# Kernel tuning notes

Hardware: AMD Instinct MI355X
Metric: run time of the kernel (lower is better)

## Reference

```python
import jax, jax.numpy as jnp
import numpy as np
from jax import lax

B, N, M = 4, 4096, 4096
DK, DQ, DV, DT, H = 3, 3, 1, 1, 64


def _mlp(x, W1, b1, W2, b2):
    # Linear -> ReLU -> Linear (weights stored as [in, out])
    return jax.nn.relu(x @ W1 + b1) @ W2 + b2


def _l1_cdist(K, Q):
    # K: [B,N,H], Q: [B,M,H] -> [B,N,M] sum_h |k-q| without a B*N*M*H intermediate.
    def step(acc, kq):
        k, q = kq  # [B,N], [B,M]
        return acc + jnp.abs(k[:, :, None] - q[:, None, :]), None
    init = jnp.zeros((K.shape[0], K.shape[1], Q.shape[1]), K.dtype)
    acc, _ = lax.scan(step, init, (jnp.moveaxis(K, -1, 0), jnp.moveaxis(Q, -1, 0)))
    return acc


def setup_inputs() -> dict:
    key = jax.random.key(0)
    ks = jax.random.split(key, 20)

    def lin(k, fan_in, fan_out):
        bound = 1.0 / np.sqrt(fan_in)
        kw, kb = jax.random.split(k)
        W = jax.random.uniform(kw, (fan_in, fan_out), jnp.float32, -bound, bound)
        b = jax.random.uniform(kb, (fan_out,), jnp.float32, -bound, bound)
        return W, b

    Wk1, bk1 = lin(ks[0], DK, H)
    Wk2, bk2 = lin(ks[1], H, H)
    Wq1, bq1 = lin(ks[2], DQ, H)
    Wq2, bq2 = lin(ks[3], H, H)
    Wv1, bv1 = lin(ks[4], DV, H)
    Wv2, bv2 = lin(ks[5], H, H)
    Wo, bo = lin(ks[6], H, DT)

    return {
        "coords_f": jax.random.normal(ks[10], (B, N, DK), jnp.float32),
        "values_f": jax.random.normal(ks[11], (B, N, DV), jnp.float32),
        "coords_t": jax.random.normal(ks[12], (B, M, DQ), jnp.float32),
        "Wk1": Wk1, "bk1": bk1, "Wk2": Wk2, "bk2": bk2,
        "Wq1": Wq1, "bq1": bq1, "Wq2": Wq2, "bq2": bq2,
        "Wv1": Wv1, "bv1": bv1, "Wv2": Wv2, "bv2": bv2,
        "Wo": Wo, "bo": bo,
    }


def reference(coords_f, values_f, coords_t,
              Wk1, bk1, Wk2, bk2,
              Wq1, bq1, Wq2, bq2,
              Wv1, bv1, Wv2, bv2,
              Wo, bo):
    K = _mlp(coords_f, Wk1, bk1, Wk2, bk2)   # [B,N,H]
    Q = _mlp(coords_t, Wq1, bq1, Wq2, bq2)   # [B,M,H]
    V = _mlp(values_f, Wv1, bv1, Wv2, bv2)   # [B,N,H]
    score = _l1_cdist(K, Q)                  # [B,N,M]
    # Gaussian kernel on L1 distance, normalized over keys (dim=1 == N axis)
    attn = jax.nn.softmax(-(score ** 2) / 2.0, axis=1)   # [B,N,M]
    out = jnp.einsum('bnm,bnh->bmh', attn, V)            # [B,M,H]
    return out @ Wo + bo                                 # [B,M,DT]
```

## Files before the change

kernel.cpp:

```cpp
#include <hip/hip_runtime.h>
#include <math.h>

#define NPTS 4096
#define CC 0.7213475204444817f

__global__ __launch_bounds__(256) void feat_kernel(
    const float* __restrict__ coords, const float* __restrict__ W1,
    const float* __restrict__ b1, const float* __restrict__ W2,
    const float* __restrict__ b2, float* __restrict__ outT, int npts)
{
  __shared__ float sW1[3 * 64], sb1[64], sW2[64 * 64], sb2[64];
  const int tid = threadIdx.x;
  for (int i = tid; i < 192; i += 256) sW1[i] = W1[i];
  if (tid < 64) { sb1[tid] = b1[tid]; sb2[tid] = b2[tid]; }
  for (int i = tid; i < 4096; i += 256) sW2[i] = W2[i];
  __syncthreads();

  const int p  = blockIdx.x * 64 + (tid & 63);
  const int qh = (tid >> 6) * 16;
  if (p >= npts) return;
  const float c0 = coords[p * 3 + 0], c1 = coords[p * 3 + 1], c2 = coords[p * 3 + 2];

  float hid[64];
  #pragma unroll
  for (int j = 0; j < 64; ++j)
    hid[j] = fmaxf(0.f, fmaf(c0, sW1[j], fmaf(c1, sW1[64 + j], fmaf(c2, sW1[128 + j], sb1[j]))));

  float acc[16];
  #pragma unroll
  for (int h = 0; h < 16; ++h) acc[h] = sb2[qh + h];
  for (int j = 0; j < 64; ++j) {
    const float hj = hid[j];
    const float4* wrow = (const float4*)&sW2[j * 64 + qh];
    #pragma unroll
    for (int hq = 0; hq < 4; ++hq) {
      float4 wv = wrow[hq];
      acc[hq * 4 + 0] = fmaf(hj, wv.x, acc[hq * 4 + 0]);
      acc[hq * 4 + 1] = fmaf(hj, wv.y, acc[hq * 4 + 1]);
      acc[hq * 4 + 2] = fmaf(hj, wv.z, acc[hq * 4 + 2]);
      acc[hq * 4 + 3] = fmaf(hj, wv.w, acc[hq * 4 + 3]);
    }
  }
  const int b = p / NPTS, n = p % NPTS;
  #pragma unroll
  for (int h = 0; h < 16; ++h)
    outT[(size_t)(b * 64 + qh + h) * NPTS + n] = acc[h];
}

__global__ __launch_bounds__(256) void vo_kernel(
    const float* __restrict__ values, const float* __restrict__ Wv1,
    const float* __restrict__ bv1, const float* __restrict__ Wv2,
    const float* __restrict__ bv2, const float* __restrict__ Wo,
    float* __restrict__ VoOut, int npts)
{
  __shared__ float sWvO[64], sW1[64], sb1[64], sc0;
  const int tid = threadIdx.x;
  if (tid < 64) {
    float a = 0.f;
    for (int h = 0; h < 64; ++h) a = fmaf(Wv2[tid * 64 + h], Wo[h], a);
    sWvO[tid] = a;
    sW1[tid] = Wv1[tid];
    sb1[tid] = bv1[tid];
  } else if (tid == 64) {
    float a = 0.f;
    for (int h = 0; h < 64; ++h) a = fmaf(bv2[h], Wo[h], a);
    sc0 = a;
  }
  __syncthreads();
  const int p = blockIdx.x * 256 + tid;
  if (p >= npts) return;
  const float v = values[p];
  float a = sc0;
  #pragma unroll 8
  for (int j = 0; j < 64; ++j)
    a = fmaf(fmaxf(0.f, fmaf(v, sW1[j], sb1[j])), sWvO[j], a);
  VoOut[p] = a;
}

__global__ void __launch_bounds__(1024)
attn_kernel(
    const float* __restrict__ Kt, const float* __restrict__ Qt,
    const float* __restrict__ Vo, const float* __restrict__ bo,
    float* __restrict__ out)
{
  __shared__ float Qs[64 * 64];
  __shared__ float MtL[1024];
  __shared__ float numL[8192];
  __shared__ float denL[8192];

  const int b    = blockIdx.x >> 6;
  const int m0   = (blockIdx.x & 63) << 6;
  const int tid  = threadIdx.x;
  const int w    = tid >> 6;
  const int lane = tid & 63;
  const int lm = lane >> 3, ln = lane & 7;

  const float* __restrict__ KtB = Kt + (size_t)b * 64 * NPTS;
  const float* __restrict__ QtB = Qt + (size_t)b * 64 * NPTS;
  const float* __restrict__ VoB = Vo + (size_t)b * NPTS;

  {
    const int h = tid >> 4, c16 = (tid & 15) * 4;
    *(float4*)&Qs[h * 64 + c16] = *(const float4*)&QtB[(size_t)h * NPTS + m0 + c16];
    #pragma unroll
    for (int j = 0; j < 8; ++j) {
      numL[w * 512 + j * 64 + lane] = 0.f;
      denL[w * 512 + j * 64 + lane] = 0.f;
    }
  }
  __syncthreads();

  float acc[32];
  float Mt[8];
  #pragma unroll
  for (int x = 0; x < 32; ++x) acc[x] = 0.f;
  #pragma unroll
  for (int j = 0; j < 8; ++j) Mt[j] = __builtin_inff();

  const float* __restrict__ Kb = KtB + w * 32 + ln * 4;
  const float* __restrict__ Qb = &Qs[lm * 8];

  for (int I = 0; I < 8; ++I) {
    const float* __restrict__ Kn = Kb + I * 512;
    #pragma unroll 2
    for (int h = 0; h < 64; ++h) {
      float q[8], k[4];
      *(float4*)&k[0] = *(const float4*)(Kn + (size_t)h * NPTS);
      *(float4*)&q[0] = *(const float4*)(Qb + h * 64);
      *(float4*)&q[4] = *(const float4*)(Qb + h * 64 + 4);
      #pragma unroll
      for (int j = 0; j < 8; ++j) {
        #pragma unroll
        for (int i = 0; i < 4; i += 2) {
          float d0, d1;
          asm("v_sub_f32 %0, %4, %6\n\t"
              "v_sub_f32 %1, %5, %6\n\t"
              "v_add_f32 %2, %2, |%0|\n\t"
              "v_add_f32 %3, %3, |%1|"
              : "=&v"(d0), "=&v"(d1),
                "+v"(acc[j * 4 + i]), "+v"(acc[j * 4 + i + 1])
              : "v"(k[i]), "v"(k[i + 1]), "v"(q[j]));
        }
      }
    }

    {
      float vo[4];
      const int vb = I * 512 + w * 32 + ln * 4;
      *(float4*)&vo[0] = *(const float4*)&VoB[vb];
      #pragma unroll
      for (int j = 0; j < 8; ++j) {
        float rmin = fminf(fminf(acc[j*4+0], acc[j*4+1]), fminf(acc[j*4+2], acc[j*4+3]));
        rmin = fminf(rmin, __shfl_xor(rmin, 1));
        rmin = fminf(rmin, __shfl_xor(rmin, 2));
        rmin = fminf(rmin, __shfl_xor(rmin, 4));
        const float nM = fminf(Mt[j], rmin * rmin);
        const float sc = __builtin_amdgcn_exp2f(CC * (nM - Mt[j]));
        const int slot = w * 512 + j * 64 + lane;
        float nm = numL[slot] * sc;
        float dn = denL[slot] * sc;
        Mt[j] = nM;
        const float base = CC * nM;
        #pragma unroll
        for (int i = 0; i < 4; ++i) {
          const float a = acc[j * 4 + i];
          const float wgt = __builtin_amdgcn_exp2f(fmaf(-CC, a * a, base));
          dn += wgt;
          nm = fmaf(wgt, vo[i], nm);
          acc[j * 4 + i] = 0.f;
        }
        numL[slot] = nm;
        denL[slot] = dn;
      }
    }
  }

  if (ln == 0) {
    #pragma unroll
    for (int j = 0; j < 8; ++j)
      MtL[w * 64 + lm * 8 + j] = Mt[j];
  }
  __syncthreads();

  if (tid < 64) {
    const int m = tid;
    float M = __builtin_inff();
    #pragma unroll
    for (int ww = 0; ww < 16; ++ww) M = fminf(M, MtL[ww * 64 + m]);
    float Ns = 0.f, Ds = 0.f;
    #pragma unroll
    for (int ww = 0; ww < 16; ++ww) {
      const float f = __builtin_amdgcn_exp2f(CC * (M - MtL[ww * 64 + m]));
      float ns = 0.f, ds = 0.f;
      #pragma unroll
      for (int l = 0; l < 8; ++l) {
        ns += numL[ww * 512 + (m & 7) * 64 + (m >> 3) * 8 + l];
        ds += denL[ww * 512 + (m & 7) * 64 + (m >> 3) * 8 + l];
      }
      Ns = fmaf(ns, f, Ns);
      Ds = fmaf(ds, f, Ds);
    }
    out[(size_t)b * NPTS + m0 + m] = Ns / Ds + bo[0];
  }
}

extern "C" void kernel_launch(void* const* d_in, const int* in_sizes, int n_in,
                              void* d_out, int out_size, void* d_ws, size_t ws_size,
                              hipStream_t stream)
{
  const float* coords_f = (const float*)d_in[0];
  const float* values_f = (const float*)d_in[1];
  const float* coords_t = (const float*)d_in[2];
  const float* Wk1 = (const float*)d_in[3];
  const float* bk1 = (const float*)d_in[4];
  const float* Wk2 = (const float*)d_in[5];
  const float* bk2 = (const float*)d_in[6];
  const float* Wq1 = (const float*)d_in[7];
  const float* bq1 = (const float*)d_in[8];
  const float* Wq2 = (const float*)d_in[9];
  const float* bq2 = (const float*)d_in[10];
  const float* Wv1 = (const float*)d_in[11];
  const float* bv1 = (const float*)d_in[12];
  const float* Wv2 = (const float*)d_in[13];
  const float* bv2 = (const float*)d_in[14];
  const float* Wo  = (const float*)d_in[15];
  const float* bo  = (const float*)d_in[16];

  const int B    = in_sizes[0] / (NPTS * 3);
  const int npts = B * NPTS;

  float* Kt  = (float*)d_ws;
  float* Qt  = Kt + (size_t)B * 64 * NPTS;
  float* VoW = Qt + (size_t)B * 64 * NPTS;

  feat_kernel<<<npts / 64, 256, 0, stream>>>(coords_f, Wk1, bk1, Wk2, bk2, Kt, npts);
  feat_kernel<<<npts / 64, 256, 0, stream>>>(coords_t, Wq1, bq1, Wq2, bq2, Qt, npts);
  vo_kernel<<<npts / 256, 256, 0, stream>>>(values_f, Wv1, bv1, Wv2, bv2, Wo, VoW, npts);
  attn_kernel<<<B * 64, 1024, 0, stream>>>(Kt, Qt, VoW, bo, (float*)d_out);
}
```

Baseline: 234.3 us.

## Quantize K/Q to fixed-point integers and use v_sad_u32 for L1 distance

The feature MLPs now write K and Q as biased fixed-point unsigned integers (scaled by 2^19, offset by 2^30). The attention inner loop accumulates the L1 distance with one v_sad_u32 per element instead of a float subtract plus abs-add pair, roughly halving the distance-loop instruction count. Row minima use unsigned compares, and the scale factor is folded into the exponent constant. The cost is quantization error in K and Q, plus overflow risk if |value|*2^19 approaches 2^30 or the 64-term sum exceeds 32 bits.

Result: faster. 225.0 us (-4.0%).

```diff
diff --git a/kernel.cpp b/kernel.cpp
--- a/kernel.cpp
+++ b/kernel.cpp
@@ -2,12 +2,17 @@
 #include <math.h>
 
 #define NPTS 4096
-#define CC 0.7213475204444817f
+#define CC  0.7213475204444817f
+#define QSC 524288.0f
+#define QIN (1.0f / 524288.0f)
+#define CCI (CC * QIN * QIN)
+
+__device__ __forceinline__ unsigned umin2(unsigned a, unsigned b) { return a < b ? a : b; }
 
 __global__ __launch_bounds__(256) void feat_kernel(
     const float* __restrict__ coords, const float* __restrict__ W1,
     const float* __restrict__ b1, const float* __restrict__ W2,
-    const float* __restrict__ b2, float* __restrict__ outT, int npts)
+    const float* __restrict__ b2, unsigned* __restrict__ outT, int npts)
 {
   __shared__ float sW1[3 * 64], sb1[64], sW2[64 * 64], sb2[64];
   const int tid = threadIdx.x;
@@ -44,7 +49,8 @@
   const int b = p / NPTS, n = p % NPTS;
   #pragma unroll
   for (int h = 0; h < 16; ++h)
-    outT[(size_t)(b * 64 + qh + h) * NPTS + n] = acc[h];
+    outT[(size_t)(b * 64 + qh + h) * NPTS + n] =
+        (unsigned)((int)rintf(acc[h] * QSC) + (1 << 30));
 }
 
 __global__ __launch_bounds__(256) void vo_kernel(
@@ -79,11 +85,11 @@
 
 __global__ void __launch_bounds__(1024)
 attn_kernel(
-    const float* __restrict__ Kt, const float* __restrict__ Qt,
+    const unsigned* __restrict__ Kt, const unsigned* __restrict__ Qt,
     const float* __restrict__ Vo, const float* __restrict__ bo,
     float* __restrict__ out)
 {
-  __shared__ float Qs[64 * 64];
+  __shared__ unsigned Qs[64 * 64];
   __shared__ float MtL[1024];
   __shared__ float numL[8192];
   __shared__ float denL[8192];
@@ -95,13 +101,13 @@
   const int lane = tid & 63;
   const int lm = lane >> 3, ln = lane & 7;
 
-  const float* __restrict__ KtB = Kt + (size_t)b * 64 * NPTS;
-  const float* __restrict__ QtB = Qt + (size_t)b * 64 * NPTS;
-  const float* __restrict__ VoB = Vo + (size_t)b * NPTS;
+  const unsigned* __restrict__ KtB = Kt + (size_t)b * 64 * NPTS;
+  const unsigned* __restrict__ QtB = Qt + (size_t)b * 64 * NPTS;
+  const float*    __restrict__ VoB = Vo + (size_t)b * NPTS;
 
   {
     const int h = tid >> 4, c16 = (tid & 15) * 4;
-    *(float4*)&Qs[h * 64 + c16] = *(const float4*)&QtB[(size_t)h * NPTS + m0 + c16];
+    *(uint4*)&Qs[h * 64 + c16] = *(const uint4*)&QtB[(size_t)h * NPTS + m0 + c16];
     #pragma unroll
     for (int j = 0; j < 8; ++j) {
       numL[w * 512 + j * 64 + lane] = 0.f;
@@ -110,36 +116,31 @@
   }
   __syncthreads();
 
-  float acc[32];
+  unsigned acc[32];
   float Mt[8];
   #pragma unroll
-  for (int x = 0; x < 32; ++x) acc[x] = 0.f;
+  for (int x = 0; x < 32; ++x) acc[x] = 0u;
   #pragma unroll
   for (int j = 0; j < 8; ++j) Mt[j] = __builtin_inff();
 
-  const float* __restrict__ Kb = KtB + w * 32 + ln * 4;
-  const float* __restrict__ Qb = &Qs[lm * 8];
+  const unsigned* __restrict__ Kb = KtB + w * 32 + ln * 4;
+  const unsigned* __restrict__ Qb = &Qs[lm * 8];
 
   for (int I = 0; I < 8; ++I) {
-    const float* __restrict__ Kn = Kb + I * 512;
+    const unsigned* __restrict__ Kn = Kb + I * 512;
     #pragma unroll 2
     for (int h = 0; h < 64; ++h) {
-      float q[8], k[4];
-      *(float4*)&k[0] = *(const float4*)(Kn + (size_t)h * NPTS);
-      *(float4*)&q[0] = *(const float4*)(Qb + h * 64);
-      *(float4*)&q[4] = *(const float4*)(Qb + h * 64 + 4);
+      unsigned q[8], k[4];
+      *(uint4*)&k[0] = *(const uint4*)(Kn + (size_t)h * NPTS);
+      *(uint4*)&q[0] = *(const uint4*)(Qb + h * 64);
+      *(uint4*)&q[4] = *(const uint4*)(Qb + h * 64 + 4);
       #pragma unroll
       for (int j = 0; j < 8; ++j) {
         #pragma unroll
-        for (int i = 0; i < 4; i += 2) {
-          float d0, d1;
-          asm("v_sub_f32 %0, %4, %6\n\t"
-              "v_sub_f32 %1, %5, %6\n\t"
-              "v_add_f32 %2, %2, |%0|\n\t"
-              "v_add_f32 %3, %3, |%1|"
-              : "=&v"(d0), "=&v"(d1),
-                "+v"(acc[j * 4 + i]), "+v"(acc[j * 4 + i + 1])
-              : "v"(k[i]), "v"(k[i + 1]), "v"(q[j]));
+        for (int i = 0; i < 4; ++i) {
+          asm("v_sad_u32 %0, %1, %2, %0"
+              : "+v"(acc[j * 4 + i])
+              : "v"(k[i]), "v"(q[j]));
         }
       }
     }
@@ -150,11 +151,12 @@
       *(float4*)&vo[0] = *(const float4*)&VoB[vb];
       #pragma unroll
       for (int j = 0; j < 8; ++j) {
-        float rmin = fminf(fminf(acc[j*4+0], acc[j*4+1]), fminf(acc[j*4+2], acc[j*4+3]));
-        rmin = fminf(rmin, __shfl_xor(rmin, 1));
-        rmin = fminf(rmin, __shfl_xor(rmin, 2));
-        rmin = fminf(rmin, __shfl_xor(rmin, 4));
-        const float nM = fminf(Mt[j], rmin * rmin);
+        unsigned rmin = umin2(umin2(acc[j*4+0], acc[j*4+1]), umin2(acc[j*4+2], acc[j*4+3]));
+        rmin = umin2(rmin, __shfl_xor(rmin, 1));
+        rmin = umin2(rmin, __shfl_xor(rmin, 2));
+        rmin = umin2(rmin, __shfl_xor(rmin, 4));
+        const float rminf = (float)rmin * QIN;
+        const float nM = fminf(Mt[j], rminf * rminf);
         const float sc = __builtin_amdgcn_exp2f(CC * (nM - Mt[j]));
         const int slot = w * 512 + j * 64 + lane;
         float nm = numL[slot] * sc;
@@ -163,11 +165,11 @@
         const float base = CC * nM;
         #pragma unroll
         for (int i = 0; i < 4; ++i) {
-          const float a = acc[j * 4 + i];
-          const float wgt = __builtin_amdgcn_exp2f(fmaf(-CC, a * a, base));
+          const float af = (float)acc[j * 4 + i];
+          const float wgt = __builtin_amdgcn_exp2f(fmaf(-CCI, af * af, base));
           dn += wgt;
           nm = fmaf(wgt, vo[i], nm);
-          acc[j * 4 + i] = 0.f;
+          acc[j * 4 + i] = 0u;
         }
         numL[slot] = nm;
         denL[slot] = dn;
@@ -229,12 +231,12 @@
   const int B    = in_sizes[0] / (NPTS * 3);
   const int npts = B * NPTS;
 
-  float* Kt  = (float*)d_ws;
-  float* Qt  = Kt + (size_t)B * 64 * NPTS;
-  float* VoW = Qt + (size_t)B * 64 * NPTS;
-
-  feat_kernel<<<npts / 64, 256, 0, stream>>>(coords_f, Wk1, bk1, Wk2, bk2, Kt, npts);
-  feat_kernel<<<npts / 64, 256, 0, stream>>>(coords_t, Wq1, bq1, Wq2, bq2, Qt, npts);
+  unsigned* KtI = (unsigned*)d_ws;
+  unsigned* QtI = KtI + (size_t)B * 64 * NPTS;
+  float*    VoW = (float*)(QtI + (size_t)B * 64 * NPTS);
+
+  feat_kernel<<<npts / 64, 256, 0, stream>>>(coords_f, Wk1, bk1, Wk2, bk2, KtI, npts);
+  feat_kernel<<<npts / 64, 256, 0, stream>>>(coords_t, Wq1, bq1, Wq2, bq2, QtI, npts);
   vo_kernel<<<npts / 256, 256, 0, stream>>>(values_f, Wv1, bv1, Wv2, bv2, Wo, VoW, npts);
-  attn_kernel<<<B * 64, 1024, 0, stream>>>(Kt, Qt, VoW, bo, (float*)d_out);
-}
+  attn_kernel<<<B * 64, 1024, 0, stream>>>(KtI, QtI, VoW, bo, (float*)d_out);
+}
```
